# Kernel optimization log

Measured on AMD Instinct MI355X. Metric: run time of the kernel, lower is better.

Reference implementation:

```python
import jax, jax.numpy as jnp
import numpy as np

C, H_IMG = 1, 1024
N_PATCH = 64
L = 12          # blocks
NH = 12         # heads
D = 768         # hidden_d
DH = D // NH    # head dim
MLP = 4 * D
OUT_D = 1000
BATCH = 256
PATCH = H_IMG // N_PATCH
IN_D = C * PATCH
SEQ = N_PATCH + 1


def _pos_emb(pos, dim):
    # faithful to original: exponent uses i directly (2*i/dim), sin for even i, cos for odd i
    p = np.arange(pos, dtype=np.float64)[:, None]
    i = np.arange(dim, dtype=np.float64)[None, :]
    ang = p / np.power(10000.0, 2.0 * i / dim)
    pe = np.where((np.arange(dim)[None, :] % 2) == 0, np.sin(ang), np.cos(ang))
    return jnp.asarray(pe, dtype=jnp.float32)


def setup_inputs() -> dict:
    key = jax.random.key(0)
    ks = jax.random.split(key, 24)
    s = lambda fan: 1.0 / np.sqrt(fan)
    inp = {
        "images": jax.random.normal(ks[0], (BATCH, C, H_IMG), jnp.float32),
        "linear_w": jax.random.uniform(ks[1], (D, IN_D), jnp.float32, -s(IN_D), s(IN_D)),
        "linear_b": jax.random.uniform(ks[2], (D,), jnp.float32, -s(IN_D), s(IN_D)),
        "class_token": jax.random.uniform(ks[3], (1, D), jnp.float32),
        "pos_emb": _pos_emb(SEQ, D),
        "ln1_g": jnp.ones((L, D), jnp.float32),
        "ln1_b": jnp.zeros((L, D), jnp.float32),
        "wq": jax.random.uniform(ks[4], (L, NH, DH, DH), jnp.float32, -s(DH), s(DH)),
        "bq": jax.random.uniform(ks[5], (L, NH, DH), jnp.float32, -s(DH), s(DH)),
        "wk": jax.random.uniform(ks[6], (L, NH, DH, DH), jnp.float32, -s(DH), s(DH)),
        "bk": jax.random.uniform(ks[7], (L, NH, DH), jnp.float32, -s(DH), s(DH)),
        "wv": jax.random.uniform(ks[8], (L, NH, DH, DH), jnp.float32, -s(DH), s(DH)),
        "bv": jax.random.uniform(ks[9], (L, NH, DH), jnp.float32, -s(DH), s(DH)),
        "ln2_g": jnp.ones((L, D), jnp.float32),
        "ln2_b": jnp.zeros((L, D), jnp.float32),
        "w1": jax.random.uniform(ks[10], (L, MLP, D), jnp.float32, -s(D), s(D)),
        "b1": jax.random.uniform(ks[11], (L, MLP), jnp.float32, -s(D), s(D)),
        "w2": jax.random.uniform(ks[12], (L, D, MLP), jnp.float32, -s(MLP), s(MLP)),
        "b2": jax.random.uniform(ks[13], (L, D), jnp.float32, -s(MLP), s(MLP)),
        "head_w": jax.random.uniform(ks[14], (OUT_D, D), jnp.float32, -s(D), s(D)),
        "head_b": jax.random.uniform(ks[15], (OUT_D,), jnp.float32, -s(D), s(D)),
    }
    return inp


def _ln(x, g, b):
    m = jnp.mean(x, axis=-1, keepdims=True)
    v = jnp.var(x, axis=-1, keepdims=True)
    return (x - m) / jnp.sqrt(v + 1e-5) * g + b


def _block(x, g1, be1, wq, bq, wk, bk, wv, bv, g2, be2, w1, bb1, w2, bb2):
    B, S, _ = x.shape
    h = _ln(x, g1, be1).reshape(B, S, NH, DH)  # split heads along feature dim
    q = jnp.einsum('bshd,hed->bshe', h, wq) + bq
    k = jnp.einsum('bshd,hed->bshe', h, wk) + bk
    v = jnp.einsum('bshd,hed->bshe', h, wv) + bv
    scores = jnp.einsum('bshe,bthe->bhst', q, k) / np.sqrt(DH).astype(np.float32)
    attn = jax.nn.softmax(scores, axis=-1)
    o = jnp.einsum('bhst,bthe->bshe', attn, v).reshape(B, S, D)
    x = x + o
    h2 = _ln(x, g2, be2)
    m = jax.nn.gelu(jnp.einsum('bsd,fd->bsf', h2, w1) + bb1, approximate=False)
    m = jnp.einsum('bsf,df->bsd', m, w2) + bb2
    return x + m


def reference(images, linear_w, linear_b, class_token, pos_emb,
              ln1_g, ln1_b, wq, bq, wk, bk, wv, bv, ln2_g, ln2_b,
              w1, b1, w2, b2, head_w, head_b):
    n = images.shape[0]
    # patchify: [n, c, h] -> [n, n_patch, c*patch_size] (flatten is (c, patch) row-major)
    patches = images.reshape(n, C, N_PATCH, PATCH).transpose(0, 2, 1, 3).reshape(n, N_PATCH, IN_D)
    tokens = jnp.einsum('npi,di->npd', patches, linear_w) + linear_b
    cls = jnp.broadcast_to(class_token[None], (n, 1, D))
    x = jnp.concatenate([cls, tokens], axis=1) + pos_emb[None]
    for l in range(L):
        x = _block(x, ln1_g[l], ln1_b[l], wq[l], bq[l], wk[l], bk[l], wv[l], bv[l],
                   ln2_g[l], ln2_b[l], w1[l], b1[l], w2[l], b2[l])
    cls_out = x[:, 0]
    logits = cls_out @ head_w.T + head_b
    return jax.nn.softmax(logits, axis=-1)
```

## Files before the change

kernel.cpp:

```cpp
#include <hip/hip_runtime.h>

#define NLAYER 12
#define NHEAD  12
#define DHEAD  64
#define DMODEL 768
#define SEQL   65
#define NBATCH 256
#define MTOK   (NBATCH*SEQL)
#define MLPD   3072

typedef _Float16 f16;
typedef f16  f16x8 __attribute__((ext_vector_type(8)));
typedef f16  f16x4 __attribute__((ext_vector_type(4)));
typedef float f32x4 __attribute__((ext_vector_type(4)));

#define MFMA(a,b,c) __builtin_amdgcn_mfma_f32_16x16x32_f16(a,b,c,0,0,0)

__device__ __forceinline__ void gload16(const void* g, void* l) {
  __builtin_amdgcn_global_load_lds((const __attribute__((address_space(1))) void*)g,
                                   (__attribute__((address_space(3))) void*)l, 16, 0, 0);
}

__global__ __launch_bounds__(256) void cvt_f16k(const float* __restrict__ in,
                                                f16* __restrict__ out, int n) {
  long i = ((long)blockIdx.x*256 + threadIdx.x)*4;
  if (i >= n) return;
  const float4 v = *(const float4*)(in + i);
  f16x4 o = { (f16)v.x, (f16)v.y, (f16)v.z, (f16)v.w };
  *(f16x4*)(out + i) = o;
}

__global__ __launch_bounds__(256) void patch_embed(
    const float* __restrict__ images, const float* __restrict__ lw,
    const float* __restrict__ lb, const float* __restrict__ cls,
    const float* __restrict__ pe, float* __restrict__ x) {
  const int s = blockIdx.x, n = blockIdx.y, tid = threadIdx.x;
  __shared__ float p[16];
  if (s > 0 && tid < 16) p[tid] = images[(long)n*1024 + (s-1)*16 + tid];
  __syncthreads();
  float* xr = x + ((long)n*SEQL + s)*DMODEL;
  #pragma unroll
  for (int j = 0; j < 3; ++j) {
    int d = tid + j*256;
    float v;
    if (s == 0) {
      v = cls[d] + pe[d];
    } else {
      float acc = lb[d];
      #pragma unroll
      for (int i = 0; i < 16; ++i) acc += p[i]*lw[d*16+i];
      v = acc + pe[s*DMODEL + d];
    }
    xr[d] = v;
  }
}

__global__ __launch_bounds__(256) void ln_kernel(
    const float* __restrict__ x, const float* __restrict__ g,
    const float* __restrict__ b, f16* __restrict__ out) {
  const int row = blockIdx.x, tid = threadIdx.x;
  const float* xr = x + (long)row*DMODEL;
  float v0 = xr[tid], v1 = xr[tid+256], v2 = xr[tid+512];
  float s = v0+v1+v2;
  float s2 = v0*v0 + v1*v1 + v2*v2;
  #pragma unroll
  for (int o = 32; o >= 1; o >>= 1) { s += __shfl_xor(s, o); s2 += __shfl_xor(s2, o); }
  __shared__ float red[8];
  const int wave = tid>>6, lane = tid&63;
  if (lane == 0) { red[wave] = s; red[4+wave] = s2; }
  __syncthreads();
  s  = red[0]+red[1]+red[2]+red[3];
  s2 = red[4]+red[5]+red[6]+red[7];
  float mean = s * (1.f/768.f);
  float var  = s2 * (1.f/768.f) - mean*mean;
  float rstd = rsqrtf(var + 1e-5f);
  f16* orow = out + (long)row*DMODEL;
  orow[tid]     = (f16)((v0-mean)*rstd*g[tid]     + b[tid]);
  orow[tid+256] = (f16)((v1-mean)*rstd*g[tid+256] + b[tid+256]);
  orow[tid+512] = (f16)((v2-mean)*rstd*g[tid+512] + b[tid+512]);
}

__global__ __launch_bounds__(256) void attn_kernel(
    const f16* __restrict__ h, const f16* __restrict__ wq, const f16* __restrict__ wk,
    const f16* __restrict__ wv, const float* __restrict__ bq, const float* __restrict__ bk,
    const float* __restrict__ bv, float* __restrict__ x) {
  __shared__ __align__(16) f16 HsPs[80*104];
  __shared__ __align__(16) f16 Qs[80*72];
  __shared__ __align__(16) f16 Ks[80*72];
  __shared__ __align__(16) f16 Vt[64*104];
  const int hd = blockIdx.x, b = blockIdx.y;
  const int tid = threadIdx.x, wave = tid>>6, lane = tid&63;
  const int lc = lane & 15, lg = lane >> 4;
  const f16* hbase = h + ((long)b*SEQL)*DMODEL + hd*DHEAD;

  for (int c = tid; c < 80*8; c += 256) {
    int s = c >> 3, ec = (c & 7)*8;
    uint4 val = {0u,0u,0u,0u};
    if (s < SEQL) val = *(const uint4*)(hbase + (long)s*DMODEL + ec);
    *(uint4*)&HsPs[s*104 + ec] = val;
  }
  for (int c = tid; c < 64*104/8; c += 256) {
    uint4 z = {0u,0u,0u,0u};
    *(uint4*)&Vt[c*8] = z;
  }
  __syncthreads();

  for (int task = wave; task < 15; task += 4) {
    int mat = task / 5, mt = task % 5;
    const f16* W = (mat == 0 ? wq : mat == 1 ? wk : wv) + hd*DHEAD*DHEAD;
    const float* bias = (mat == 0 ? bq : mat == 1 ? bk : bv) + hd*DHEAD;
    #pragma unroll
    for (int nt = 0; nt < 4; ++nt) {
      f32x4 a = {0.f,0.f,0.f,0.f};
      #pragma unroll
      for (int kt = 0; kt < 2; ++kt) {
        f16x8 af = *(const f16x8*)&HsPs[(mt*16 + lc)*104 + kt*32 + lg*8];
        f16x8 bf = *(const f16x8*)&W[(nt*16 + lc)*DHEAD + kt*32 + lg*8];
        a = MFMA(af, bf, a);
      }
      float bb = bias[nt*16 + lc];
      #pragma unroll
      for (int r = 0; r < 4; ++r) {
        int s = mt*16 + lg*4 + r;
        int e = nt*16 + lc;
        float v = a[r] + bb;
        if (mat == 0)      Qs[s*72 + e] = (f16)v;
        else if (mat == 1) Ks[s*72 + e] = (f16)v;
        else               Vt[e*104 + s] = (f16)v;
      }
    }
  }
  __syncthreads();

  for (int mt = wave; mt < 5; mt += 4) {
    {
      uint2 z = {0u,0u};
      *(uint2*)&HsPs[(mt*16 + (lane>>2))*104 + 80 + (lane&3)*4] = z;
    }
    f32x4 sc[5];
    #pragma unroll
    for (int nt = 0; nt < 5; ++nt) {
      f32x4 a = {0.f,0.f,0.f,0.f};
      #pragma unroll
      for (int kt = 0; kt < 2; ++kt) {
        f16x8 af = *(const f16x8*)&Qs[(mt*16 + lc)*72 + kt*32 + lg*8];
        f16x8 bf = *(const f16x8*)&Ks[(nt*16 + lc)*72 + kt*32 + lg*8];
        a = MFMA(af, bf, a);
      }
      sc[nt] = a;
    }
    #pragma unroll
    for (int r = 0; r < 4; ++r) {
      float vals[5];
      #pragma unroll
      for (int nt = 0; nt < 5; ++nt) {
        float v = sc[nt][r]*0.125f;
        if (nt*16 + lc > 64) v = -1e30f;
        vals[nt] = v;
      }
      float mx = vals[0];
      #pragma unroll
      for (int nt = 1; nt < 5; ++nt) mx = fmaxf(mx, vals[nt]);
      #pragma unroll
      for (int o = 8; o >= 1; o >>= 1) mx = fmaxf(mx, __shfl_xor(mx, o, 16));
      float sum = 0.f, p[5];
      #pragma unroll
      for (int nt = 0; nt < 5; ++nt) { p[nt] = __expf(vals[nt]-mx); sum += p[nt]; }
      #pragma unroll
      for (int o = 8; o >= 1; o >>= 1) sum += __shfl_xor(sum, o, 16);
      float inv = 1.f/sum;
      int row = mt*16 + lg*4 + r;
      #pragma unroll
      for (int nt = 0; nt < 5; ++nt) HsPs[row*104 + nt*16 + lc] = (f16)(p[nt]*inv);
    }
    f32x4 oacc[4];
    #pragma unroll
    for (int nt = 0; nt < 4; ++nt) {
      f32x4 a = {0.f,0.f,0.f,0.f};
      #pragma unroll
      for (int kt = 0; kt < 3; ++kt) {
        f16x8 af = *(const f16x8*)&HsPs[(mt*16 + lc)*104 + kt*32 + lg*8];
        f16x8 bf = *(const f16x8*)&Vt[(nt*16 + lc)*104 + kt*32 + lg*8];
        a = MFMA(af, bf, a);
      }
      oacc[nt] = a;
    }
    float* xb = x + ((long)b*SEQL)*DMODEL + hd*DHEAD;
    #pragma unroll
    for (int nt = 0; nt < 4; ++nt) {
      #pragma unroll
      for (int r = 0; r < 4; ++r) {
        int s = mt*16 + lg*4 + r;
        if (s < SEQL) {
          int e = nt*16 + lc;
          xb[(long)s*DMODEL + e] += oacc[nt][r];
        }
      }
    }
  }
}

template<int ACT>
__global__ __launch_bounds__(256) void gemm_bt(
    const f16* __restrict__ A, const f16* __restrict__ B,
    const float* __restrict__ bias, void* __restrict__ Cout,
    int M, int N, int K) {
  __shared__ __align__(16) f16 As[3][128*32];
  __shared__ __align__(16) f16 Bs[3][128*32];
  const int tid = threadIdx.x;
  const int wave = tid >> 6, lane = tid & 63;
  const int lrow = lane & 15, lk = lane >> 4;

  const int gx = gridDim.x;
  const int nwg = gx * gridDim.y;
  const int orig = blockIdx.y * gx + blockIdx.x;
  const int q = nwg >> 3, r = nwg & 7;
  const int xcd = orig & 7, lin = orig >> 3;
  const int wgid = (xcd < r ? xcd*(q+1) : r*(q+1) + (xcd - r)*q) + lin;
  const int bx = wgid % gx, by = wgid / gx;

  const long m0 = (long)by * 128, n0 = (long)bx * 128;
  const int wm = (wave >> 1) * 64, wn = (wave & 1) * 64;
  f32x4 acc[4][4];
  #pragma unroll
  for (int i = 0; i < 4; ++i)
    #pragma unroll
    for (int j = 0; j < 4; ++j) acc[i][j] = (f32x4){0.f,0.f,0.f,0.f};

  const int NT = K >> 5;
  auto stage = [&](int slot, int t) {
    const int k0 = t << 5;
    #pragma unroll
    for (int i = 0; i < 2; ++i) {
      int ch = (i*4 + wave)*64 + lane;
      int row = ch >> 2, kp = (ch & 3)*8;
      gload16(A + (m0 + row)*(long)K + k0 + kp, &As[slot][ch*8]);
      gload16(B + (n0 + row)*(long)K + k0 + kp, &Bs[slot][ch*8]);
    }
  };
  stage(0, 0);
  stage(1, 1);
  int slot = 0;
  for (int t = 0; t < NT; ++t) {
    if (t < NT-1) asm volatile("s_waitcnt vmcnt(4)" ::: "memory");
    else          asm volatile("s_waitcnt vmcnt(0)" ::: "memory");
    asm volatile("s_barrier" ::: "memory");
    if (t + 2 < NT) { int ns = slot + 2; if (ns >= 3) ns -= 3; stage(ns, t+2); }
    f16x8 af[4], bfr[4];
    #pragma unroll
    for (int i = 0; i < 4; ++i) af[i]  = *(const f16x8*)&As[slot][(wm + i*16 + lrow)*32 + lk*8];
    #pragma unroll
    for (int j = 0; j < 4; ++j) bfr[j] = *(const f16x8*)&Bs[slot][(wn + j*16 + lrow)*32 + lk*8];
    #pragma unroll
    for (int i = 0; i < 4; ++i)
      #pragma unroll
      for (int j = 0; j < 4; ++j)
        acc[i][j] = MFMA(af[i], bfr[j], acc[i][j]);
    slot = slot + 1; if (slot >= 3) slot = 0;
  }
  #pragma unroll
  for (int j = 0; j < 4; ++j) {
    int col = (int)n0 + wn + j*16 + lrow;
    float bv = bias[col];
    #pragma unroll
    for (int i = 0; i < 4; ++i) {
      #pragma unroll
      for (int r2 = 0; r2 < 4; ++r2) {
        long row = m0 + wm + i*16 + lk*4 + r2;
        float v = acc[i][j][r2] + bv;
        if (ACT == 0) {
          float g = 0.5f*v*(1.f + erff(v*0.70710678118654752f));
          ((f16*)Cout)[row*(long)N + col] = (f16)g;
        } else {
          ((float*)Cout)[row*(long)N + col] += v;
        }
      }
    }
  }
}

__global__ __launch_bounds__(256) void head_kernel(
    const float* __restrict__ x, const float* __restrict__ hw,
    const float* __restrict__ hb, float* __restrict__ out) {
  const int b = blockIdx.x, tid = threadIdx.x;
  __shared__ float cls[768];
  __shared__ float red[8];
  const float* xr = x + (long)b*SEQL*DMODEL;
  #pragma unroll
  for (int j = 0; j < 3; ++j) cls[tid + j*256] = xr[tid + j*256];
  __syncthreads();
  float lgv[4];
  #pragma unroll
  for (int j = 0; j < 4; ++j) {
    int c = tid + j*256;
    float acc = -1e30f;
    if (c < 1000) {
      const float* wr = hw + (long)c*768;
      float s_ = 0.f;
      for (int i = 0; i < 768; ++i) s_ += cls[i]*wr[i];
      acc = s_ + hb[c];
    }
    lgv[j] = acc;
  }
  const int wave = tid>>6, lane = tid&63;
  float mx = fmaxf(fmaxf(lgv[0],lgv[1]),fmaxf(lgv[2],lgv[3]));
  #pragma unroll
  for (int o = 32; o >= 1; o >>= 1) mx = fmaxf(mx, __shfl_xor(mx, o));
  if (lane == 0) red[wave] = mx;
  __syncthreads();
  mx = fmaxf(fmaxf(red[0],red[1]),fmaxf(red[2],red[3]));
  float e[4]; float sum = 0.f;
  #pragma unroll
  for (int j = 0; j < 4; ++j) {
    int c = tid + j*256;
    e[j] = (c < 1000) ? expf(lgv[j]-mx) : 0.f;
    sum += e[j];
  }
  #pragma unroll
  for (int o = 32; o >= 1; o >>= 1) sum += __shfl_xor(sum, o);
  if (lane == 0) red[4+wave] = sum;
  __syncthreads();
  sum = red[4]+red[5]+red[6]+red[7];
  float inv = 1.f/sum;
  #pragma unroll
  for (int j = 0; j < 4; ++j) {
    int c = tid + j*256;
    if (c < 1000) out[(long)b*1000 + c] = e[j]*inv;
  }
}

extern "C" void kernel_launch(void* const* d_in, const int* in_sizes, int n_in,
                              void* d_out, int out_size, void* d_ws, size_t ws_size,
                              hipStream_t stream) {
  const float* images     = (const float*)d_in[0];
  const float* linear_w   = (const float*)d_in[1];
  const float* linear_b   = (const float*)d_in[2];
  const float* class_tok  = (const float*)d_in[3];
  const float* pos_emb    = (const float*)d_in[4];
  const float* ln1_g      = (const float*)d_in[5];
  const float* ln1_b      = (const float*)d_in[6];
  const float* wq         = (const float*)d_in[7];
  const float* bq         = (const float*)d_in[8];
  const float* wk         = (const float*)d_in[9];
  const float* bk         = (const float*)d_in[10];
  const float* wv         = (const float*)d_in[11];
  const float* bv         = (const float*)d_in[12];
  const float* ln2_g      = (const float*)d_in[13];
  const float* ln2_b      = (const float*)d_in[14];
  const float* w1         = (const float*)d_in[15];
  const float* b1         = (const float*)d_in[16];
  const float* w2         = (const float*)d_in[17];
  const float* b2         = (const float*)d_in[18];
  const float* head_w     = (const float*)d_in[19];
  const float* head_b     = (const float*)d_in[20];

  char* ws = (char*)d_ws;
  float* xbuf = (float*)(ws + 0);
  f16*   hbuf = (f16*)(ws + 51118080);
  f16*   mbuf = (f16*)(ws + 76677120);
  f16*   w1all = (f16*)(ws + 178913280);
  f16*   w2all = (f16*)(ws + 235536384);
  f16*   wqbB  = (f16*)(ws + 292159488);
  f16*   wkbB  = (f16*)(ws + 293339136);
  f16*   wvbB  = (f16*)(ws + 294518784);
  f16*   w1b  = (f16*)(ws + 178913280);
  f16*   w2b  = (f16*)(ws + 183631872);
  f16*   wqbS = (f16*)(ws + 188350464);
  f16*   wkbS = (f16*)(ws + 189530112);
  f16*   wvbS = (f16*)(ws + 190709760);
  if (ws_size < 191889408ull) return;
  const bool big = ws_size >= 295698432ull;
  f16* wqb = big ? wqbB : wqbS;
  f16* wkb = big ? wkbB : wkbS;
  f16* wvb = big ? wvbB : wvbS;

  patch_embed<<<dim3(SEQL, NBATCH), 256, 0, stream>>>(images, linear_w, linear_b,
                                                      class_tok, pos_emb, xbuf);
  cvt_f16k<<<576, 256, 0, stream>>>(wq, wqb, 589824);
  cvt_f16k<<<576, 256, 0, stream>>>(wk, wkb, 589824);
  cvt_f16k<<<576, 256, 0, stream>>>(wv, wvb, 589824);
  if (big) {
    cvt_f16k<<<27648, 256, 0, stream>>>(w1, w1all, 28311552);
    cvt_f16k<<<27648, 256, 0, stream>>>(w2, w2all, 28311552);
  }

  for (int l = 0; l < NLAYER; ++l) {
    ln_kernel<<<MTOK, 256, 0, stream>>>(xbuf, ln1_g + l*768, ln1_b + l*768, hbuf);
    attn_kernel<<<dim3(NHEAD, NBATCH), 256, 0, stream>>>(
        hbuf, wqb + l*49152, wkb + l*49152, wvb + l*49152,
        bq + l*768, bk + l*768, bv + l*768, xbuf);
    ln_kernel<<<MTOK, 256, 0, stream>>>(xbuf, ln2_g + l*768, ln2_b + l*768, hbuf);
    f16* w1p = big ? (w1all + (long)l*2359296) : w1b;
    f16* w2p = big ? (w2all + (long)l*2359296) : w2b;
    if (!big) cvt_f16k<<<2304, 256, 0, stream>>>(w1 + (long)l*2359296, w1b, 2359296);
    gemm_bt<0><<<dim3(MLPD/128, MTOK/128), 256, 0, stream>>>(
        hbuf, w1p, b1 + l*3072, (void*)mbuf, MTOK, MLPD, DMODEL);
    if (!big) cvt_f16k<<<2304, 256, 0, stream>>>(w2 + (long)l*2359296, w2b, 2359296);
    gemm_bt<1><<<dim3(DMODEL/128, MTOK/128), 256, 0, stream>>>(
        mbuf, w2p, b2 + l*768, (void*)xbuf, MTOK, DMODEL, MLPD);
  }
  head_kernel<<<NBATCH, 256, 0, stream>>>(xbuf, head_w, head_b, (float*)d_out);
}
```

Baseline: 5.434 ms.

## Replace MLP GEMM with 256x256-tile 512-thread kernel using swizzled LDS

The MLP GEMM now uses 256x256 output tiles with 8 waves per workgroup instead of 128x128 tiles with 4 waves. It adds a 4-slot LDS ring buffer with an XOR-swizzled layout to avoid bank conflicts. The A and B prefetches are split across two half-iterations, each bracketed by barriers, and MFMA priority is raised with s_setprio. The larger tiles raise data reuse per LDS load. The cost is far fewer workgroups: the second GEMM (N=768) launches only 195 blocks, fewer than there are CUs, and the larger LDS footprint limits residency.

```diff
diff --git a/kernel.cpp b/kernel.cpp
--- a/kernel.cpp
+++ b/kernel.cpp
@@ -201,15 +201,16 @@
 }
 
 template<int ACT>
-__global__ __launch_bounds__(256) void gemm_bt(
+__global__ __launch_bounds__(512, 2) void gemm256(
     const f16* __restrict__ A, const f16* __restrict__ B,
     const float* __restrict__ bias, void* __restrict__ Cout,
     int M, int N, int K) {
-  __shared__ __align__(16) f16 As[3][128*32];
-  __shared__ __align__(16) f16 Bs[3][128*32];
+  __shared__ __align__(16) f16 As[4][256*32];
+  __shared__ __align__(16) f16 Bs[4][256*32];
   const int tid = threadIdx.x;
-  const int wave = tid >> 6, lane = tid & 63;
+  const int wid = tid >> 6, lane = tid & 63;
   const int lrow = lane & 15, lk = lane >> 4;
+  const int wr = wid >> 2, wc = wid & 3;
 
   const int gx = gridDim.x;
   const int nwg = gx * gridDim.y;
@@ -219,55 +220,92 @@
   const int wgid = (xcd < r ? xcd*(q+1) : r*(q+1) + (xcd - r)*q) + lin;
   const int bx = wgid % gx, by = wgid / gx;
 
-  const long m0 = (long)by * 128, n0 = (long)bx * 128;
-  const int wm = (wave >> 1) * 64, wn = (wave & 1) * 64;
-  f32x4 acc[4][4];
-  #pragma unroll
-  for (int i = 0; i < 4; ++i)
+  const long m0 = (long)by * 256, n0 = (long)bx * 256;
+
+  f32x4 acc[8][4];
+  #pragma unroll
+  for (int i = 0; i < 8; ++i)
     #pragma unroll
     for (int j = 0; j < 4; ++j) acc[i][j] = (f32x4){0.f,0.f,0.f,0.f};
 
   const int NT = K >> 5;
-  auto stage = [&](int slot, int t) {
-    const int k0 = t << 5;
+  auto stageA = [&](int t) {
+    const int s = t & 3;
     #pragma unroll
     for (int i = 0; i < 2; ++i) {
-      int ch = (i*4 + wave)*64 + lane;
-      int row = ch >> 2, kp = (ch & 3)*8;
-      gload16(A + (m0 + row)*(long)K + k0 + kp, &As[slot][ch*8]);
-      gload16(B + (n0 + row)*(long)K + k0 + kp, &Bs[slot][ch*8]);
+      int c = tid + i*512;
+      int row = c >> 2;
+      int kp = (c & 3) ^ ((row >> 1) & 3);
+      gload16(A + (m0 + row)*(long)K + t*32 + kp*8, &As[s][c*8]);
     }
   };
-  stage(0, 0);
-  stage(1, 1);
-  int slot = 0;
+  auto stageB = [&](int t) {
+    const int s = t & 3;
+    #pragma unroll
+    for (int i = 0; i < 2; ++i) {
+      int c = tid + i*512;
+      int row = c >> 2;
+      int kp = (c & 3) ^ ((row >> 1) & 3);
+      gload16(B + (n0 + row)*(long)K + t*32 + kp*8, &Bs[s][c*8]);
+    }
+  };
+
+  stageA(0); stageB(0);
+  if (NT > 1) { stageA(1); stageB(1); }
+
   for (int t = 0; t < NT; ++t) {
-    if (t < NT-1) asm volatile("s_waitcnt vmcnt(4)" ::: "memory");
-    else          asm volatile("s_waitcnt vmcnt(0)" ::: "memory");
+    const int s = t & 3;
+    if (t + 2 < NT) asm volatile("s_waitcnt vmcnt(4)" ::: "memory");
+    else            asm volatile("s_waitcnt vmcnt(0)" ::: "memory");
     asm volatile("s_barrier" ::: "memory");
-    if (t + 2 < NT) { int ns = slot + 2; if (ns >= 3) ns -= 3; stage(ns, t+2); }
-    f16x8 af[4], bfr[4];
-    #pragma unroll
-    for (int i = 0; i < 4; ++i) af[i]  = *(const f16x8*)&As[slot][(wm + i*16 + lrow)*32 + lk*8];
-    #pragma unroll
-    for (int j = 0; j < 4; ++j) bfr[j] = *(const f16x8*)&Bs[slot][(wn + j*16 + lrow)*32 + lk*8];
-    #pragma unroll
-    for (int i = 0; i < 4; ++i)
-      #pragma unroll
-      for (int j = 0; j < 4; ++j)
-        acc[i][j] = MFMA(af[i], bfr[j], acc[i][j]);
-    slot = slot + 1; if (slot >= 3) slot = 0;
-  }
-  #pragma unroll
-  for (int j = 0; j < 4; ++j) {
-    int col = (int)n0 + wn + j*16 + lrow;
+
+    if (t + 2 < NT) stageA(t + 2);
+    f16x8 bf[4], af[4];
+    #pragma unroll
+    for (int nf = 0; nf < 4; ++nf) {
+      int row = wc*64 + nf*16 + lrow;
+      bf[nf] = *(const f16x8*)&Bs[s][row*32 + ((lk ^ ((row>>1)&3))*8)];
+    }
+    #pragma unroll
+    for (int mf = 0; mf < 4; ++mf) {
+      int row = wr*128 + mf*16 + lrow;
+      af[mf] = *(const f16x8*)&As[s][row*32 + ((lk ^ ((row>>1)&3))*8)];
+    }
+    __builtin_amdgcn_s_setprio(1);
+    #pragma unroll
+    for (int mf = 0; mf < 4; ++mf)
+      #pragma unroll
+      for (int nf = 0; nf < 4; ++nf)
+        acc[mf][nf] = MFMA(af[mf], bf[nf], acc[mf][nf]);
+    __builtin_amdgcn_s_setprio(0);
+    asm volatile("s_barrier" ::: "memory");
+
+    if (t + 2 < NT) stageB(t + 2);
+    #pragma unroll
+    for (int mf = 0; mf < 4; ++mf) {
+      int row = wr*128 + 64 + mf*16 + lrow;
+      af[mf] = *(const f16x8*)&As[s][row*32 + ((lk ^ ((row>>1)&3))*8)];
+    }
+    __builtin_amdgcn_s_setprio(1);
+    #pragma unroll
+    for (int mf = 0; mf < 4; ++mf)
+      #pragma unroll
+      for (int nf = 0; nf < 4; ++nf)
+        acc[4+mf][nf] = MFMA(af[mf], bf[nf], acc[4+mf][nf]);
+    __builtin_amdgcn_s_setprio(0);
+    asm volatile("s_barrier" ::: "memory");
+  }
+
+  #pragma unroll
+  for (int nf = 0; nf < 4; ++nf) {
+    int col = (int)n0 + wc*64 + nf*16 + lrow;
     float bv = bias[col];
     #pragma unroll
-    for (int i = 0; i < 4; ++i) {
+    for (int mf = 0; mf < 8; ++mf) {
       #pragma unroll
       for (int r2 = 0; r2 < 4; ++r2) {
-        long row = m0 + wm + i*16 + lk*4 + r2;
-        float v = acc[i][j][r2] + bv;
+        long row = m0 + wr*128 + mf*16 + lk*4 + r2;
+        float v = acc[mf][nf][r2] + bv;
         if (ACT == 0) {
           float g = 0.5f*v*(1.f + erff(v*0.70710678118654752f));
           ((f16*)Cout)[row*(long)N + col] = (f16)g;
@@ -393,10 +431,10 @@
     f16* w1p = big ? (w1all + (long)l*2359296) : w1b;
     f16* w2p = big ? (w2all + (long)l*2359296) : w2b;
     if (!big) cvt_f16k<<<2304, 256, 0, stream>>>(w1 + (long)l*2359296, w1b, 2359296);
-    gemm_bt<0><<<dim3(MLPD/128, MTOK/128), 256, 0, stream>>>(
+    gemm256<0><<<dim3(MLPD/256, MTOK/256), 512, 0, stream>>>(
         hbuf, w1p, b1 + l*3072, (void*)mbuf, MTOK, MLPD, DMODEL);
     if (!big) cvt_f16k<<<2304, 256, 0, stream>>>(w2 + (long)l*2359296, w2b, 2359296);
-    gemm_bt<1><<<dim3(DMODEL/128, MTOK/128), 256, 0, stream>>>(
+    gemm256<1><<<dim3(DMODEL/256, MTOK/256), 512, 0, stream>>>(
         mbuf, w2p, b2 + l*768, (void*)xbuf, MTOK, DMODEL, MLPD);
   }
   head_kernel<<<NBATCH, 256, 0, stream>>>(xbuf, head_w, head_b, (float*)d_out);
```

Result: slower. 6.011 ms (+10.6%).
